# Kernel optimization log

Hardware: AMD Instinct MI355X
Metric: run time of the kernel (lower is better)

Reference implementation:

```python
import jax, jax.numpy as jnp
import numpy as np

K_F = 3
NUM = K_F * K_F - 1          # 8 non-center neighbors
IDX_REF = NUM // 2           # 4 (center insertion index)
PROP_TIME = 18
AFFINITY_GAMMA = 0.5
B, H, W = 4, 480, 640


def _bilinear(img, y, x):
    """Bilinear sample img [H,W] at float coords y,x [K,H,W]; zero outside."""
    Hh, Ww = img.shape
    y0 = jnp.floor(y)
    x0 = jnp.floor(x)

    def gather(yy, xx):
        valid = (yy >= 0) & (yy < Hh) & (xx >= 0) & (xx < Ww)
        yi = jnp.clip(yy.astype(jnp.int32), 0, Hh - 1)
        xi = jnp.clip(xx.astype(jnp.int32), 0, Ww - 1)
        return jnp.where(valid, img[yi, xi], 0.0)

    wy = y - y0
    wx = x - x0
    return ((1 - wy) * (1 - wx) * gather(y0, x0)
            + (1 - wy) * wx * gather(y0, x0 + 1)
            + wy * (1 - wx) * gather(y0 + 1, x0)
            + wy * wx * gather(y0 + 1, x0 + 1))


def _deform_prop(feat, dy, dx, aff):
    """Modulated deformable 3x3 conv with all-ones weight, zero bias, ch=1.
    feat [B,1,H,W]; dy,dx,aff [B,9,H,W]. Output = sum_k aff_k * sample_k."""
    b, _, h, w = feat.shape
    ky = jnp.array([-1, -1, -1, 0, 0, 0, 1, 1, 1], feat.dtype)
    kx = jnp.array([-1, 0, 1, -1, 0, 1, -1, 0, 1], feat.dtype)
    gy = jnp.arange(h, dtype=feat.dtype)[:, None]   # [H,1]
    gx = jnp.arange(w, dtype=feat.dtype)[None, :]   # [1,W]
    py = gy[None, None] + ky[None, :, None, None] + dy  # [B,9,H,W]
    px = gx[None, None] + kx[None, :, None, None] + dx
    samp = jax.vmap(_bilinear)(feat[:, 0], py, px)      # [B,9,H,W]
    return jnp.sum(samp * aff, axis=1, keepdims=True)


def _affinity_normalization(aff, scale):
    # TGASS: tanh / (gamma*num), abs-sum normalize (clamped at 1), reference = 1 - sum
    aff = jnp.tanh(aff) / (scale + 1e-8)
    s = jnp.sum(jnp.abs(aff), axis=1, keepdims=True) + 1e-4
    s = jnp.maximum(s, 1.0)
    aff = aff / s
    aff_ref = 1.0 - jnp.sum(aff, axis=1, keepdims=True)
    return jnp.concatenate([aff[:, :IDX_REF], aff_ref, aff[:, IDX_REF:]], axis=1)


def setup_inputs() -> dict:
    key = jax.random.key(0)
    k1, k2, k3, k4, k5 = jax.random.split(key, 5)
    feat_init = jax.random.uniform(k1, (B, 1, H, W), jnp.float32) * 10.0
    guidance = jax.random.normal(k2, (B, 24, H, W), jnp.float32)
    confidence = jax.random.uniform(k3, (B, 1, H, W), jnp.float32)
    dense = jax.random.uniform(k4, (B, 1, H, W), jnp.float32) * 10.0
    mask = (jax.random.uniform(k5, (B, 1, H, W)) < 0.05).astype(jnp.float32)
    feat_fix = dense * mask
    aff_scale_const = jnp.full((1,), AFFINITY_GAMMA * NUM, jnp.float32)
    return {"feat_init": feat_init, "guidance": guidance,
            "confidence": confidence, "feat_fix": feat_fix,
            "aff_scale_const": aff_scale_const}


def reference(feat_init, guidance, confidence, feat_fix, aff_scale_const):
    b = feat_init.shape[0]
    h, w = feat_init.shape[2], feat_init.shape[3]
    # offsets: chunk guidance into (o1, o2, aff), interleave, insert zero at center
    o1, o2, aff_g = jnp.split(guidance, 3, axis=1)
    off = jnp.concatenate([o1, o2], axis=1).reshape(b, NUM, 2, h, w)
    zc = jnp.zeros((b, 1, 2, h, w), off.dtype)
    off = jnp.concatenate([off[:, :IDX_REF], zc, off[:, IDX_REF:]], axis=1)
    dy, dx = off[:, :, 0], off[:, :, 1]          # [B,9,H,W]
    aff = _affinity_normalization(aff_g, aff_scale_const)

    # preserve_input: fixed-pixel mask (ch_f == 1)
    mask_fix = (feat_fix > 0.0).astype(feat_init.dtype)
    conf = (1.0 - mask_fix) * confidence + mask_fix
    feat = (1.0 - mask_fix) * feat_init + mask_fix * feat_fix

    def step(f, _):
        f = _deform_prop(f * conf, dy, dx, aff)
        f = (1.0 - mask_fix) * f + mask_fix * feat_fix
        return f, None

    feat, _ = jax.lax.scan(step, feat, None, length=PROP_TIME)
    return feat
```

## Files before the change

kernel.cpp:

```cpp
#include <hip/hip_runtime.h>


#define HH 480
#define WW 640
#define BB 4
#define HWSZ (HH * WW)
#define NPIX (BB * HWSZ)
#define PROP_T 18
#define SLACK 704

struct f2u { float x, y; };

__device__ __forceinline__ float fast_tanh(float x) {
    x = fminf(fmaxf(x, -15.0f), 15.0f);
    float e = __expf(2.0f * x);
    return __fdividef(e - 1.0f, e + 1.0f);
}

__global__ __launch_bounds__(256) void precompute_kernel(
    const float* __restrict__ feat_init,
    const float* __restrict__ confidence,
    const float* __restrict__ feat_fix,
    float* __restrict__ g0,
    float2* __restrict__ ac_mid,
    float2* __restrict__ ac_last) {
    int p = blockIdx.x * 256 + threadIdx.x;
    if (p >= NPIX) return;
    float ff = feat_fix[p];
    float m  = (ff > 0.0f) ? 1.0f : 0.0f;
    float km = 1.0f - m;
    float conf = km * confidence[p] + m;
    float f0   = km * feat_init[p] + m * ff;
    g0[p] = f0 * conf;
    ac_mid[p]  = make_float2(conf * km, conf * m * ff);
    ac_last[p] = make_float2(km, m * ff);
}

__global__ __launch_bounds__(256) void step_kernel(
    const float* __restrict__ fin,
    float* __restrict__ fout,
    const float* __restrict__ guid,
    const float* __restrict__ aff_scale,
    const float2* __restrict__ ac) {
    const int x = blockIdx.x * 64 + threadIdx.x;
    const int y = blockIdx.y * 4 + threadIdx.y;
    const int b = blockIdx.z;
    const int q = y * WW + x;
    const int pix = b * HWSZ + q;
    const float* gb = guid + (size_t)b * 24 * HWSZ + q;

    const float inv_scale = __fdividef(1.0f, aff_scale[0] + 1e-8f);
    float t[8];
    float ssum = 1e-4f;
#pragma unroll
    for (int j = 0; j < 8; ++j) {
        float v = fast_tanh(gb[(16 + j) * HWSZ]) * inv_scale;
        t[j] = v;
        ssum += fabsf(v);
    }
    ssum = fmaxf(ssum, 1.0f);
    float rs = __fdividef(1.0f, ssum);
    float asum = 0.0f;
#pragma unroll
    for (int j = 0; j < 8; ++j) { t[j] *= rs; asum += t[j]; }
    const float aref = 1.0f - asum;

    const float* fb = fin + b * HWSZ;
    const float yf = (float)y, xf = (float)x;
    float acc = 0.0f;

    constexpr int KY[9] = {-1, -1, -1, 0, 0, 0, 1, 1, 1};
    constexpr int KX[9] = {-1, 0, 1, -1, 0, 1, -1, 0, 1};
#pragma unroll
    for (int k = 0; k < 9; ++k) {
        float dy, dx, ak;
        if (k == 4) {
            dy = 0.0f; dx = 0.0f; ak = aref;
        } else {
            const int n = (k < 4) ? k : (k - 1);
            dy = gb[(2 * n) * HWSZ];
            dx = gb[(2 * n + 1) * HWSZ];
            ak = t[n];
        }
        float py = yf + (float)KY[k] + dy;
        float px = xf + (float)KX[k] + dx;
        float y0f = floorf(py), x0f = floorf(px);
        float wy = py - y0f, wx = px - x0f;
        int y0 = (int)y0f, x0 = (int)x0f;
        float vy0 = (y0 >= 0 && y0 < HH) ? 1.0f : 0.0f;
        float vy1 = (y0 >= -1 && y0 < HH - 1) ? 1.0f : 0.0f;
        float vx0 = (x0 >= 0 && x0 < WW) ? 1.0f : 0.0f;
        float vx1 = (x0 >= -1 && x0 < WW - 1) ? 1.0f : 0.0f;
        float omwy = 1.0f - wy, omwx = 1.0f - wx;
        float w00 = omwy * omwx * vy0 * vx0 * ak;
        float w01 = omwy * wx  * vy0 * vx1 * ak;
        float w10 = wy * omwx  * vy1 * vx0 * ak;
        float w11 = wy * wx    * vy1 * vx1 * ak;
        int yc = min(max(y0, -1), HH - 1);
        int xc = min(max(x0, -1), WW - 1);
        int idx = yc * WW + xc;
        f2u r0 = *reinterpret_cast<const f2u*>(fb + idx);
        f2u r1 = *reinterpret_cast<const f2u*>(fb + idx + WW);
        acc += w00 * r0.x + w01 * r0.y + w10 * r1.x + w11 * r1.y;
    }

    float2 c2 = ac[pix];
    fout[pix] = c2.x * acc + c2.y;
}

extern "C" void kernel_launch(void* const* d_in, const int* in_sizes, int n_in,
                              void* d_out, int out_size, void* d_ws, size_t ws_size,
                              hipStream_t stream) {
    const float* feat_init  = (const float*)d_in[0];
    const float* guidance   = (const float*)d_in[1];
    const float* confidence = (const float*)d_in[2];
    const float* feat_fix   = (const float*)d_in[3];
    const float* aff_scale  = (const float*)d_in[4];

    const size_t bufFloats = (size_t)NPIX + 2 * SLACK;
    float* bufA = (float*)d_ws;
    float* bufB = bufA + bufFloats;
    float2* acMid  = (float2*)(bufB + bufFloats);
    float2* acLast = acMid + NPIX;
    float* fA = bufA + SLACK;
    float* fB = bufB + SLACK;

    hipMemsetAsync(bufA, 0, bufFloats * sizeof(float), stream);
    hipMemsetAsync(bufB, 0, bufFloats * sizeof(float), stream);

    precompute_kernel<<<NPIX / 256, 256, 0, stream>>>(
        feat_init, confidence, feat_fix, fA, acMid, acLast);

    dim3 blk(64, 4, 1);
    dim3 grd(WW / 64, HH / 4, BB);
    for (int t = 0; t < PROP_T; ++t) {
        const float* fin = (t & 1) ? fB : fA;
        float* fout = (t == PROP_T - 1) ? (float*)d_out : ((t & 1) ? fA : fB);
        const float2* ac = (t == PROP_T - 1) ? acLast : acMid;
        step_kernel<<<grd, blk, 0, stream>>>(fin, fout, guidance, aff_scale, ac);
    }
}
```

Measured before the change: 713.9 us.

## Precompute bilinear gather indices and fp16 weights once, reuse across propagation steps

```diff
diff --git a/kernel.cpp b/kernel.cpp
--- a/kernel.cpp
+++ b/kernel.cpp
@@ -1,4 +1,5 @@
 #include <hip/hip_runtime.h>
+#include <hip/hip_fp16.h>
 
 
 #define HH 480
@@ -19,35 +20,32 @@
 
 __global__ __launch_bounds__(256) void precompute_kernel(
     const float* __restrict__ feat_init,
+    const float* __restrict__ guid,
     const float* __restrict__ confidence,
     const float* __restrict__ feat_fix,
+    const float* __restrict__ aff_scale,
     float* __restrict__ g0,
     float2* __restrict__ ac_mid,
-    float2* __restrict__ ac_last) {
-    int p = blockIdx.x * 256 + threadIdx.x;
-    if (p >= NPIX) return;
-    float ff = feat_fix[p];
-    float m  = (ff > 0.0f) ? 1.0f : 0.0f;
-    float km = 1.0f - m;
-    float conf = km * confidence[p] + m;
-    float f0   = km * feat_init[p] + m * ff;
-    g0[p] = f0 * conf;
-    ac_mid[p]  = make_float2(conf * km, conf * m * ff);
-    ac_last[p] = make_float2(km, m * ff);
-}
-
-__global__ __launch_bounds__(256) void step_kernel(
-    const float* __restrict__ fin,
-    float* __restrict__ fout,
-    const float* __restrict__ guid,
-    const float* __restrict__ aff_scale,
-    const float2* __restrict__ ac) {
+    float2* __restrict__ ac_last,
+    int* __restrict__ idxArr,
+    uint2* __restrict__ wArr) {
     const int x = blockIdx.x * 64 + threadIdx.x;
     const int y = blockIdx.y * 4 + threadIdx.y;
     const int b = blockIdx.z;
     const int q = y * WW + x;
     const int pix = b * HWSZ + q;
     const float* gb = guid + (size_t)b * 24 * HWSZ + q;
+
+    {
+        float ff = feat_fix[pix];
+        float m  = (ff > 0.0f) ? 1.0f : 0.0f;
+        float km = 1.0f - m;
+        float conf = km * confidence[pix] + m;
+        float f0   = km * feat_init[pix] + m * ff;
+        g0[pix] = f0 * conf;
+        ac_mid[pix]  = make_float2(conf * km, conf * m * ff);
+        ac_last[pix] = make_float2(km, m * ff);
+    }
 
     const float inv_scale = __fdividef(1.0f, aff_scale[0] + 1e-8f);
     float t[8];
@@ -65,10 +63,7 @@
     for (int j = 0; j < 8; ++j) { t[j] *= rs; asum += t[j]; }
     const float aref = 1.0f - asum;
 
-    const float* fb = fin + b * HWSZ;
     const float yf = (float)y, xf = (float)x;
-    float acc = 0.0f;
-
     constexpr int KY[9] = {-1, -1, -1, 0, 0, 0, 1, 1, 1};
     constexpr int KX[9] = {-1, 0, 1, -1, 0, 1, -1, 0, 1};
 #pragma unroll
@@ -98,12 +93,37 @@
         float w11 = wy * wx    * vy1 * vx1 * ak;
         int yc = min(max(y0, -1), HH - 1);
         int xc = min(max(x0, -1), WW - 1);
-        int idx = yc * WW + xc;
-        f2u r0 = *reinterpret_cast<const f2u*>(fb + idx);
-        f2u r1 = *reinterpret_cast<const f2u*>(fb + idx + WW);
-        acc += w00 * r0.x + w01 * r0.y + w10 * r1.x + w11 * r1.y;
+        int idx = b * HWSZ + yc * WW + xc;
+
+        idxArr[k * NPIX + pix] = idx;
+        __half2 hab = __floats2half2_rn(w00, w01);
+        __half2 hcd = __floats2half2_rn(w10, w11);
+        uint2 wr;
+        wr.x = *reinterpret_cast<unsigned int*>(&hab);
+        wr.y = *reinterpret_cast<unsigned int*>(&hcd);
+        wArr[k * NPIX + pix] = wr;
     }
+}
 
+__global__ __launch_bounds__(256) void step_kernel(
+    const float* __restrict__ fin,
+    float* __restrict__ fout,
+    const int* __restrict__ idxArr,
+    const uint2* __restrict__ wArr,
+    const float2* __restrict__ ac) {
+    const int pix = blockIdx.x * 256 + threadIdx.x;
+    float acc = 0.0f;
+#pragma unroll
+    for (int k = 0; k < 9; ++k) {
+        int idx = idxArr[k * NPIX + pix];
+        uint2 wr = wArr[k * NPIX + pix];
+        const float* p = fin + idx;
+        f2u r0 = *reinterpret_cast<const f2u*>(p);
+        f2u r1 = *reinterpret_cast<const f2u*>(p + WW);
+        float2 wab = __half22float2(*reinterpret_cast<__half2*>(&wr.x));
+        float2 wcd = __half22float2(*reinterpret_cast<__half2*>(&wr.y));
+        acc += wab.x * r0.x + wab.y * r0.y + wcd.x * r1.x + wcd.y * r1.y;
+    }
     float2 c2 = ac[pix];
     fout[pix] = c2.x * acc + c2.y;
 }
@@ -122,21 +142,26 @@
     float* bufB = bufA + bufFloats;
     float2* acMid  = (float2*)(bufB + bufFloats);
     float2* acLast = acMid + NPIX;
+    int*   idxArr  = (int*)(acLast + NPIX);
+    uint2* wArr    = (uint2*)(idxArr + 9 * (size_t)NPIX);
     float* fA = bufA + SLACK;
     float* fB = bufB + SLACK;
 
     hipMemsetAsync(bufA, 0, bufFloats * sizeof(float), stream);
     hipMemsetAsync(bufB, 0, bufFloats * sizeof(float), stream);
 
-    precompute_kernel<<<NPIX / 256, 256, 0, stream>>>(
-        feat_init, confidence, feat_fix, fA, acMid, acLast);
+    {
+        dim3 blk(64, 4, 1);
+        dim3 grd(WW / 64, HH / 4, BB);
+        precompute_kernel<<<grd, blk, 0, stream>>>(
+            feat_init, guidance, confidence, feat_fix, aff_scale,
+            fA, acMid, acLast, idxArr, wArr);
+    }
 
-    dim3 blk(64, 4, 1);
-    dim3 grd(WW / 64, HH / 4, BB);
     for (int t = 0; t < PROP_T; ++t) {
         const float* fin = (t & 1) ? fB : fA;
         float* fout = (t == PROP_T - 1) ? (float*)d_out : ((t & 1) ? fA : fB);
         const float2* ac = (t == PROP_T - 1) ? acLast : acMid;
-        step_kernel<<<grd, blk, 0, stream>>>(fin, fout, guidance, aff_scale, ac);
+        step_kernel<<<NPIX / 256, 256, 0, stream>>>(fin, fout, idxArr, wArr, ac);
     }
 }
```

Result: slower. 766.7 us (+7.4%).
